# Kernel optimization log

Hardware: AMD Instinct MI355X
Metric: run time of the kernel (lower is better)

The kernel has to match this reference:

```python
import jax, jax.numpy as jnp
import numpy as np
from jax import lax

EPS = 1e-7
MAX_NORM = 1.0 - 1e-5

# ---- Poincare ball (c=1) primitives ----

def _norm(x):
    return jnp.sqrt(jnp.sum(x * x, -1, keepdims=True) + EPS)

def proj(x):
    n = _norm(x)
    return x * jnp.minimum(1.0, MAX_NORM / n)

def expmap0(v):
    n = _norm(v)
    return jnp.tanh(n) * v / n

def logmap0(x):
    n = _norm(x)
    return jnp.arctanh(jnp.clip(n, 0.0, MAX_NORM)) * x / n

def mobius_add(u, v):
    uv = jnp.sum(u * v, -1, keepdims=True)
    uu = jnp.sum(u * u, -1, keepdims=True)
    vv = jnp.sum(v * v, -1, keepdims=True)
    num = (1.0 + 2.0 * uv + vv) * u + (1.0 - uu) * v
    den = 1.0 + 2.0 * uv + uu * vv
    return num / den

# Mobius matvec M (x) x = expmap0(logmap0(x) @ M^T)

def gru_step(h, x, Wr, Wz, Wh, Ur, Uz, Uh, br, bz, bh):
    lh = logmap0(h)
    lx = logmap0(x)
    r = jax.nn.sigmoid(logmap0(mobius_add(mobius_add(expmap0(lh @ Wr.T), expmap0(lx @ Ur.T)), br)))
    z = jax.nn.sigmoid(logmap0(mobius_add(mobius_add(expmap0(lh @ Wz.T), expmap0(lx @ Uz.T)), bz)))
    htil = mobius_add(mobius_add(expmap0((r * lh) @ Wh.T), expmap0(lx @ Uh.T)), bh)
    delta = mobius_add(-h, htil)
    return proj(mobius_add(h, expmap0(z * logmap0(delta))))


def hyperplane_logits(X, P, A):
    # Hyperbolic MLR (Ganea et al.) without materializing [N,V,d]:
    # (-p)(+)x = (-alpha*p + beta*x) / gamma
    xx = jnp.sum(X * X, -1)                  # [N]
    pp = jnp.sum(P * P, -1)                  # [V]
    aa = jnp.sqrt(jnp.sum(A * A, -1) + EPS)  # [V]
    pa = jnp.sum(P * A, -1)                  # [V]
    px = X @ P.T                             # [N,V]
    xa = X @ A.T                             # [N,V]
    alpha = 1.0 - 2.0 * px + xx[:, None]
    beta = (1.0 - pp)[None, :]
    gamma = 1.0 - 2.0 * px + pp[None, :] * xx[:, None]
    da = (-alpha * pa[None, :] + beta * xa) / gamma
    dd = (alpha * alpha * pp[None, :] - 2.0 * alpha * beta * px + beta * beta * xx[:, None]) / (gamma * gamma)
    lam = 2.0 / (1.0 - pp)                   # conformal factor at p_k
    arg = 2.0 * da / ((1.0 - dd) * aa[None, :] + EPS)
    return (lam * aa)[None, :] * jnp.arcsinh(arg)


VOCAB, EMB, HID, LAYERS = 10000, 512, 512, 3
B, S = 16, 128


def setup_inputs() -> dict:
    key = jax.random.key(0)
    ks = jax.random.split(key, 16)
    inp = jax.random.randint(ks[0], (B, S), 0, VOCAB)
    tgt = jax.random.randint(ks[1], (B, S), 0, VOCAB)
    E = proj(0.01 * jax.random.normal(ks[2], (VOCAB, EMB), jnp.float32))
    E = E.at[0].set(0.0)  # padding_idx=0
    mk = lambda k: 0.05 * jax.random.normal(k, (LAYERS, HID, HID), jnp.float32)
    Wr, Wz, Wh = mk(ks[3]), mk(ks[4]), mk(ks[5])
    Ur, Uz, Uh = mk(ks[6]), mk(ks[7]), mk(ks[8])
    mb = lambda k: proj(0.01 * jax.random.normal(k, (LAYERS, HID), jnp.float32))
    br, bz, bh = mb(ks[9]), mb(ks[10]), mb(ks[11])
    P = proj(0.01 * jax.random.normal(ks[12], (VOCAB, HID), jnp.float32))
    A = 0.05 * jax.random.normal(ks[13], (VOCAB, HID), jnp.float32)
    return {"input": inp, "target": tgt, "E": E, "Wr": Wr, "Wz": Wz, "Wh": Wh,
            "Ur": Ur, "Uz": Uz, "Uh": Uh, "br": br, "bz": bz, "bh": bh, "P": P, "A": A}


def reference(input, target, E, Wr, Wz, Wh, Ur, Uz, Uh, br, bz, bh, P, A):
    b, s = input.shape
    x = E[input]                       # [B,S,H] points on the ball
    x = jnp.transpose(x, (1, 0, 2))    # [S,B,H]
    for l in range(LAYERS):
        params = (Wr[l], Wz[l], Wh[l], Ur[l], Uz[l], Uh[l],
                  br[l][None, :], bz[l][None, :], bh[l][None, :])
        def step(h, xt, params=params):
            h = gru_step(h, xt, *params)
            return h, h
        h0 = jnp.zeros((b, HID), x.dtype)
        _, x = lax.scan(step, h0, x)   # [S,B,H]
    X = x.transpose(1, 0, 2).reshape(-1, HID)          # [B*S,H]
    logits = hyperplane_logits(X, P, A)                # [B*S,V]
    logp = jax.nn.log_softmax(logits, axis=-1)
    nll = -jnp.take_along_axis(logp, target.reshape(-1, 1), axis=1)[:, 0]
    return jnp.mean(nll).reshape(1)
```

## Files before the change

kernel.cpp:

```cpp
#include <hip/hip_runtime.h>
#include <hip/hip_bf16.h>
#include <math.h>

#define EPSF 1e-7f
#define MAXNRM 0.99999f

static constexpr int Bb = 16, Ss = 128, Hh = 512, Vv = 10000, Ll = 3;
static constexpr int Nn = Bb * Ss;
static constexpr int VT = 625;

typedef __attribute__((ext_vector_type(4))) float f32x4;
typedef __attribute__((ext_vector_type(8))) short short8v;
typedef _Float16 h2 __attribute__((ext_vector_type(2)));

__device__ inline float4 ld4(const float* p){ return *(const float4*)p; }
__device__ inline void st4(float* p, float4 v){ *(float4*)p = v; }
__device__ inline float dot4(float4 a, float4 b){ return a.x*b.x + a.y*b.y + a.z*b.z + a.w*b.w; }
__device__ inline float sigm(float x){ return 1.f/(1.f + expf(-x)); }
__device__ inline unsigned short f2bf(float f){
  __hip_bfloat16 h = __float2bfloat16(f);
  return __builtin_bit_cast(unsigned short, h);
}
__device__ inline unsigned short f2h(float f){
  _Float16 h = (_Float16)f;
  return __builtin_bit_cast(unsigned short, h);
}
__device__ inline float rsum64f(float v){
  v+=__shfl_xor(v,32); v+=__shfl_xor(v,16); v+=__shfl_xor(v,8);
  v+=__shfl_xor(v,4);  v+=__shfl_xor(v,2);  v+=__shfl_xor(v,1); return v;
}
__device__ inline float dot4_e5m2(uint u, h2 L0, h2 L1, float acc){
  uint p01 = __builtin_amdgcn_perm(u, 0u, 0x05000400u);
  uint p23 = __builtin_amdgcn_perm(u, 0u, 0x07000600u);
  acc = __builtin_amdgcn_fdot2(__builtin_bit_cast(h2,p01), L0, acc, false);
  acc = __builtin_amdgcn_fdot2(__builtin_bit_cast(h2,p23), L1, acc, false);
  return acc;
}
__device__ inline void stg_sc(float* p, float v){
  asm volatile("global_store_dword %0, %1, off sc0 sc1" :: "v"(p), "v"(v) : "memory");
}
__device__ inline float ldg_sc1(const float* p){
  float r;
  asm volatile("global_load_dword %0, %1, off sc0 sc1\n\ts_waitcnt vmcnt(0)"
               : "=v"(r) : "v"(p) : "memory");
  return r;
}

__device__ __forceinline__ void stream_e5m2_pair(const uint* __restrict__ WA,
    const uint* __restrict__ WB, const uint* src2, float (*part)[Hh], int tid, int j8){
  int hf = tid >> 9;
  int kq = (tid >> 6) & 7;
  const uint* W = (hf ? WB : WA) + (size_t)(kq*16)*Hh + j8;
  float acc[8] = {0,0,0,0,0,0,0,0};
  #pragma unroll 4
  for(int i=0;i<16;i++){
    uint4 wa = *(const uint4*)(W + (size_t)i*Hh);
    uint4 wb = *(const uint4*)(W + (size_t)i*Hh + 4);
    uint2 L = *(const uint2*)&src2[(kq*16+i)*2];
    h2 L0=__builtin_bit_cast(h2,L.x), L1=__builtin_bit_cast(h2,L.y);
    acc[0]=dot4_e5m2(wa.x,L0,L1,acc[0]); acc[1]=dot4_e5m2(wa.y,L0,L1,acc[1]);
    acc[2]=dot4_e5m2(wa.z,L0,L1,acc[2]); acc[3]=dot4_e5m2(wa.w,L0,L1,acc[3]);
    acc[4]=dot4_e5m2(wb.x,L0,L1,acc[4]); acc[5]=dot4_e5m2(wb.y,L0,L1,acc[5]);
    acc[6]=dot4_e5m2(wb.z,L0,L1,acc[6]); acc[7]=dot4_e5m2(wb.w,L0,L1,acc[7]);
  }
  float* d = &part[hf*8+kq][j8];
  *(f32x4*)d = (f32x4){acc[0],acc[1],acc[2],acc[3]};
  *(f32x4*)(d+4) = (f32x4){acc[4],acc[5],acc[6],acc[7]};
}
__device__ __forceinline__ void stream_f16_16(const uint* __restrict__ W2, const uint* src2,
    float (*part)[Hh], int tid, int j8){
  int ks = tid >> 6;
  int kp0 = ks*16;
  const uint* W = W2 + (size_t)kp0*Hh + j8;
  f32x4 a0 = {0,0,0,0}, a1 = {0,0,0,0};
  #pragma unroll 4
  for(int kk=0; kk<16; kk++){
    uint4 wa = *(const uint4*)(W + (size_t)kk*Hh);
    uint4 wb = *(const uint4*)(W + (size_t)kk*Hh + 4);
    h2 lv = __builtin_bit_cast(h2, src2[kp0+kk]);
    a0[0]=__builtin_amdgcn_fdot2(__builtin_bit_cast(h2,wa.x), lv, a0[0], false);
    a0[1]=__builtin_amdgcn_fdot2(__builtin_bit_cast(h2,wa.y), lv, a0[1], false);
    a0[2]=__builtin_amdgcn_fdot2(__builtin_bit_cast(h2,wa.z), lv, a0[2], false);
    a0[3]=__builtin_amdgcn_fdot2(__builtin_bit_cast(h2,wa.w), lv, a0[3], false);
    a1[0]=__builtin_amdgcn_fdot2(__builtin_bit_cast(h2,wb.x), lv, a1[0], false);
    a1[1]=__builtin_amdgcn_fdot2(__builtin_bit_cast(h2,wb.y), lv, a1[1], false);
    a1[2]=__builtin_amdgcn_fdot2(__builtin_bit_cast(h2,wb.z), lv, a1[2], false);
    a1[3]=__builtin_amdgcn_fdot2(__builtin_bit_cast(h2,wb.w), lv, a1[3], false);
  }
  float* d = &part[ks][j8];
  *(f32x4*)d = a0; *(f32x4*)(d+4) = a1;
}

__global__ __launch_bounds__(256) void k_packWh(const float* __restrict__ Wh, uint* __restrict__ W2){
  int jt = blockIdx.x, kt2 = blockIdx.y, l = blockIdx.z;
  const float* src = Wh + (size_t)l*Hh*Hh;
  uint* dst = W2 + (size_t)l*(256*Hh);
  __shared__ float t[64][65];
  int tid = threadIdx.x;
  #pragma unroll
  for(int p=0;p<4;p++){
    int row = p*16 + (tid>>4);
    int c4 = (tid&15)*4;
    st4(&t[row][c4], ld4(src + ((size_t)(jt*64+row))*Hh + kt2*64 + c4));
  }
  __syncthreads();
  int kp_l = tid >> 3;
  int j8 = (tid & 7)*8;
  uint u[8];
  #pragma unroll
  for(int i=0;i<8;i++){
    int jl = j8 + i;
    u[i] = (uint)f2h(t[jl][2*kp_l]) | ((uint)f2h(t[jl][2*kp_l+1]) << 16);
  }
  uint* o = dst + (size_t)(kt2*32 + kp_l)*Hh + jt*64 + j8;
  *(uint4*)(o)   = make_uint4(u[0],u[1],u[2],u[3]);
  *(uint4*)(o+4) = make_uint4(u[4],u[5],u[6],u[7]);
}

__global__ __launch_bounds__(256) void k_packW8(const float* __restrict__ Wr,
    const float* __restrict__ Wz, uint* __restrict__ W8){
  int jt = blockIdx.x, kt = blockIdx.y, lm = blockIdx.z;
  int l = lm>>1, m = lm&1;
  const float* src = (m==0?Wr:Wz) + (size_t)l*Hh*Hh;
  uint* dst = W8 + (size_t)lm*(128*Hh);
  __shared__ float t[64][65];
  int tid = threadIdx.x;
  #pragma unroll
  for(int p=0;p<4;p++){
    int row = p*16 + (tid>>4);
    int c4 = (tid&15)*4;
    st4(&t[row][c4], ld4(src + ((size_t)(jt*64+row))*Hh + kt*64 + c4));
  }
  __syncthreads();
  #pragma unroll
  for(int p=0;p<4;p++){
    int k4l = p*4 + (tid>>6);
    int j_l = tid & 63;
    uint u = 0;
    #pragma unroll
    for(int i=0;i<4;i++){
      ushort b16 = __builtin_bit_cast(ushort, (_Float16)t[j_l][k4l*4+i]);
      uint b8 = (uint)((ushort)(b16 + 0x80) >> 8);
      u |= b8 << (8*i);
    }
// ... 69 lines not shown
  float4 v = ld4(Xp + (size_t)n*Hh + t*4);
  float ss = dot4(v,v);
  for(int o=32;o;o>>=1) ss += __shfl_down(ss,o);
  if((t&63)==0) sred[t>>6] = ss;
  __syncthreads();
  ss = sred[0]+sred[1];
  float nn = sqrtf(ss + EPSF);
  float sc = tanhf(nn) / nn;
  v.x*=sc; v.y*=sc; v.z*=sc; v.w*=sc;
  st4(Xp + (size_t)n*Hh + t*4, v);
}

__global__ __launch_bounds__(256) void k_gemm(const float* __restrict__ A4,
    const float* __restrict__ U0, const float* __restrict__ U1, const float* __restrict__ U2,
    float* __restrict__ O0, float* __restrict__ O1, float* __restrict__ O2){
  __shared__ float As[16][65], Bs[16][65];
  int jb = blockIdx.x;
  int nb = blockIdx.y;
  int mat = jb >> 3; int j0 = (jb & 7)*64;
  const float* Bm = mat==0?U0 : (mat==1?U1:U2);
  float* Om       = mat==0?O0 : (mat==1?O1:O2);
  int tid = threadIdx.x;
  int lr = tid >> 2, lq = tid & 3;
  int tx = tid & 15, ty = tid >> 4;
  float acc[4][4] = {};
  for(int kb=0; kb<Hh; kb+=16){
    float4 av = ld4(A4 + (size_t)(nb*64+lr)*Hh + kb + lq*4);
    float4 bv = ld4(Bm + (size_t)(j0+lr)*Hh + kb + lq*4);
    As[lq*4+0][lr]=av.x; As[lq*4+1][lr]=av.y; As[lq*4+2][lr]=av.z; As[lq*4+3][lr]=av.w;
    Bs[lq*4+0][lr]=bv.x; Bs[lq*4+1][lr]=bv.y; Bs[lq*4+2][lr]=bv.z; Bs[lq*4+3][lr]=bv.w;
    __syncthreads();
    #pragma unroll
    for(int kk=0;kk<16;kk++){
      float a0=As[kk][ty*4+0], a1=As[kk][ty*4+1], a2=As[kk][ty*4+2], a3=As[kk][ty*4+3];
      float b0=Bs[kk][tx*4+0], b1=Bs[kk][tx*4+1], b2=Bs[kk][tx*4+2], b3=Bs[kk][tx*4+3];
      acc[0][0]+=a0*b0; acc[0][1]+=a0*b1; acc[0][2]+=a0*b2; acc[0][3]+=a0*b3;
      acc[1][0]+=a1*b0; acc[1][1]+=a1*b1; acc[1][2]+=a1*b2; acc[1][3]+=a1*b3;
      acc[2][0]+=a2*b0; acc[2][1]+=a2*b1; acc[2][2]+=a2*b2; acc[2][3]+=a2*b3;
      acc[3][0]+=a3*b0; acc[3][1]+=a3*b1; acc[3][2]+=a3*b2; acc[3][3]+=a3*b3;
    }
    __syncthreads();
  }
  for(int i=0;i<4;i++)
    for(int j2=0;j2<4;j2++)
      Om[(size_t)(nb*64+ty*4+i)*Hh + j0 + tx*4 + j2] = acc[i][j2];
}

__global__ __launch_bounds__(1024) void k_mega(
    const float* __restrict__ XR, const float* __restrict__ XZ, const float* __restrict__ XH,
    const float* __restrict__ pubX,
    const uint* __restrict__ W8, const uint* __restrict__ W2h,
    const uint* __restrict__ U8, const uint* __restrict__ U2h,
    const float* __restrict__ brA, const float* __restrict__ bzA, const float* __restrict__ bhA,
    float* __restrict__ bnd0, float* __restrict__ bnd1,
    int* __restrict__ flags0, int* __restrict__ flags1,
    float* __restrict__ Xfin){
  const int xcd = blockIdx.x & 7;
  const int layer = xcd >> 1;
  if(layer >= 3) return;
  const int b = (xcd & 1)*8 + (blockIdx.x >> 3);
  const int tid = threadIdx.x;
  const int lane = tid & 63, wv = tid >> 6;
  const int j8 = lane * 8;

  const uint* W8r = W8 + (size_t)(layer*2+0)*128*Hh;
  const uint* W8z = W8 + (size_t)(layer*2+1)*128*Hh;
  const uint* Wh2 = W2h + (size_t)layer*256*Hh;
  const uint* U8r = U8 + (size_t)(layer*2+0)*128*Hh;
  const uint* U8z = U8 + (size_t)(layer*2+1)*128*Hh;
  const uint* Uh2 = U2h + (size_t)layer*256*Hh;
  const float* br = brA + layer*Hh;
  const float* bz = bzA + layer*Hh;
  const float* bh = bhA + layer*Hh;
  float* outX = (layer==0)? bnd0 : (layer==1)? bnd1 : Xfin;
  int* outF = (layer==0)? flags0 : (layer==1)? flags1 : nullptr;
  const float* inX = (layer==1)? bnd0 : bnd1;
  int* inF = (layer==1)? flags0 : flags1;

  __shared__ float part[16][Hh];
  __shared__ float mr_s[Hh], mur_s[Hh];
  __shared__ uint  lh2_s[256], ap2_s[256], lx2_s[256];
  __shared__ float bias0[Hh], bias1[Hh], bias2[Hh];
  __shared__ float partA[8][16];
  __shared__ float partB[8][18];
  __shared__ float coefA_s[12], coefB_s[8], bb_s[4];

  if(tid<256) lh2_s[tid]=0u;
  for(int i=tid;i<Hh;i+=1024){ bias0[i]=br[i]; bias1[i]=bz[i]; bias2[i]=bh[i]; }
  __syncthreads();
  {
    float p0=0,p1=0,p2=0;
    if(tid<Hh){ float a=bias0[tid],b2=bias1[tid],c2=bias2[tid]; p0=a*a; p1=b2*b2; p2=c2*c2; }
    p0=rsum64f(p0); p1=rsum64f(p1); p2=rsum64f(p2);
    if(tid<Hh && lane==0){ partB[wv][0]=p0; partB[wv][1]=p1; partB[wv][2]=p2; }
    __syncthreads();
    if(tid==0){
      float a=0,b2=0,c2=0;
      for(int i=0;i<8;i++){ a+=partB[i][0]; b2+=partB[i][1]; c2+=partB[i][2]; }
      bb_s[0]=a; bb_s[1]=b2; bb_s[2]=c2;
    }
    __syncthreads();
  }

  float h = 0.f;
  float Sh = 0.f, hxh = 0.f, hbh = 0.f;

  for(int ts=0; ts<Ss; ts++){
    const size_t row = (size_t)(ts*Bb + b)*Hh;

    if(layer == 0){
      float xr=0,xz=0,xh=0;
      if(tid<512){ xr=XR[row+tid]; xz=XZ[row+tid]; xh=XH[row+tid]; }
      stream_e5m2_pair(W8r, W8z, lh2_s, part, tid, j8);
      __syncthreads();
      float mr=0.f, mz=0.f;
      if(tid<512){
        float s0=0, s1=0;
        #pragma unroll
        for(int q=0;q<8;q++){ s0+=part[q][tid]; s1+=part[8+q][tid]; }
        mr=s0; mz=s1; mr_s[tid]=s0;
        float brc=bias0[tid], bzc=bias1[tid], bhc=bias2[tid];
        float p0=mr*mr, p1=mr*xr, p2=mr*brc, p3=mz*mz, p4=mz*xz, p5=mz*bzc, p6=h*xh, p7=h*bhc;
        p0=rsum64f(p0); p1=rsum64f(p1); p2=rsum64f(p2); p3=rsum64f(p3);
        p4=rsum64f(p4); p5=rsum64f(p5); p6=rsum64f(p6); p7=rsum64f(p7);
        if(lane==0){
          partA[wv][0]=p0; partA[wv][1]=p1; partA[wv][2]=p2; partA[wv][3]=p3;
          partA[wv][4]=p4; partA[wv][5]=p5; partA[wv][6]=p6; partA[wv][7]=p7;
        }
      }
      __syncthreads();
      if(tid==0){
        float s[8];
        #pragma unroll
        for(int d=0;d<8;d++){
          float x=0;
          for(int i=0;i<8;i++) x+=partA[i][d];
          s[d]=x;
        }
        hxh=s[6]; hbh=s[7];
        const float* px = pubX + (size_t)(ts*Bb+b)*6;
        float xrxr=px[0], xrbr=px[1], xzxz=px[2], xzbz=px[3];
        float bbr=bb_s[0], bbz=bb_s[1];
        float nm=sqrtf(s[0]+EPSF), se=tanhf(nm)/nm;
        float uv=se*s[1], uu=se*se*s[0];
        float den=1.f+2.f*uv+uu*xrxr;
        float a1=(1.f+2.f*uv+xrxr)*se/den, a2=(1.f-uu)/den;
        float uv2=a1*s[2]+a2*xrbr;
        float uu2=a1*a1*s[0]+2.f*a1*a2*s[1]+a2*a2*xrxr;
        float den2=1.f+2.f*uv2+uu2*bbr;
        float b1=(1.f+2.f*uv2+bbr)/den2, b2c=(1.f-uu2)/den2;
        float c1=b1*a1, c2=b1*a2, c3=b2c;
        float n2sq=c1*c1*s[0]+c2*c2*xrxr+c3*c3*bbr+2.f*(c1*c2*s[1]+c1*c3*s[2]+c2*c3*xrbr);
        float nn2=sqrtf(n2sq+EPSF);
        float s_r=atanhf(fminf(nn2,MAXNRM))/nn2;
        coefA_s[0]=s_r*c1; coefA_s[1]=s_r*c2; coefA_s[2]=s_r*c3;
        float nmz=sqrtf(s[3]+EPSF), sez=tanhf(nmz)/nmz;
        float uvz=sez*s[4], uuz=sez*sez*s[3];
        float denz=1.f+2.f*uvz+uuz*xzxz;
        float az1=(1.f+2.f*uvz+xzxz)*sez/denz, az2=(1.f-uuz)/denz;
        float uvz2=az1*s[5]+az2*xzbz;
        float uuz2=az1*az1*s[3]+2.f*az1*az2*s[4]+az2*az2*xzxz;
// ... 51 lines not shown
        float Ghh=dsum[4], Ghm=dsum[5], Ghx=dsum[6], Ghb=dsum[7];
        float Gmm=dsum[8], Gmx=dsum[9], Gmb=dsum[10];
        float Gxx=dsum[11], Gxb=dsum[12], Gbb=dsum[13];
        float Heh=dsum[14], Hem=dsum[15], Hex=dsum[16], Heb=dsum[17];
        float xhxh=coefA_s[7], xhbh=coefA_s[8];
        float bbh=bb_s[2]; float Shb=Sh;
        float nm3=sqrtf(d0+EPSF), se3=tanhf(nm3)/nm3;
        float uvh=se3*d1, uuh=se3*se3*d0;
        float denh=1.f+2.f*uvh+uuh*xhxh;
        float a1p=(1.f+2.f*uvh+xhxh)*se3/denh, a2p=(1.f-uuh)/denh;
        float uv2h=a1p*d2+a2p*xhbh;
        float uu2h=a1p*a1p*d0+2.f*a1p*a2p*d1+a2p*a2p*xhxh;
        float den2h=1.f+2.f*uv2h+uu2h*bbh;
        float b1p=(1.f+2.f*uv2h+bbh)/den2h, b2p=(1.f-uu2h)/den2h;
        float c1p=b1p*a1p, c2p=b1p*a2p, c3p=b2p;
        float h_htil=c1p*d3+c2p*hxh+c3p*hbh;
        float htil2=c1p*c1p*d0+c2p*c2p*xhxh+c3p*c3p*bbh
                  +2.f*(c1p*c2p*d1+c1p*c3p*d2+c2p*c3p*xhbh);
        float denD=1.f-2.f*h_htil+Shb*htil2;
        float dd1=(1.f-2.f*h_htil+htil2)/denD, dd2=(1.f-Shb)/denD;
        float g0=-dd1, g1=dd2*c1p, g2=dd2*c2p, g3=dd2*c3p;
        float del2=g0*g0*Shb+g1*g1*d0+g2*g2*xhxh+g3*g3*bbh
                 +2.f*(g0*g1*d3+g0*g2*hxh+g0*g3*hbh+g1*g2*d1+g1*g3*d2+g2*g3*xhbh);
        float ndl=sqrtf(del2+EPSF);
        float sld=atanhf(fminf(ndl,MAXNRM))/ndl;
        float Qe=g0*g0*Ghh+g1*g1*Gmm+g2*g2*Gxx+g3*g3*Gbb
               +2.f*(g0*g1*Ghm+g0*g2*Ghx+g0*g3*Ghb+g1*g2*Gmx+g1*g3*Gmb+g2*g3*Gxb);
        float Le=g0*Heh+g1*Hem+g2*Hex+g3*Heb;
        float Sww=sld*sld*Qe;
        float Shw=sld*Le;
        float nw=sqrtf(Sww+EPSF), sew=tanhf(nw)/nw;
        float uvw=sew*Shw, vvw=sew*sew*Sww;
        float denw=1.f+2.f*uvw+Shb*vvw;
        float q1=(1.f+2.f*uvw+vvw)/denw, q2=((1.f-Shb)/denw)*sew;
        float n2h=q1*q1*Shb+2.f*q1*q2*Shw+q2*q2*Sww;
        float nrm=sqrtf(n2h+EPSF);
        float scl=fminf(1.f, MAXNRM/nrm);
        float Shn=scl*scl*n2h;
        float nh2=sqrtf(Shn+EPSF);
        float slh=atanhf(fminf(nh2,MAXNRM))/nh2;
        coefB_s[0]=scl*q1; coefB_s[1]=scl*q2*sld;
        coefB_s[2]=g0; coefB_s[3]=g1; coefB_s[4]=g2; coefB_s[5]=g3;
        coefB_s[6]=slh;
        Sh=Shn;
      }
      __syncthreads();
      if(tid<512){
        float qc1=coefB_s[0], qc2=coefB_s[1];
        float g0=coefB_s[2], g1=coefB_s[3], g2=coefB_s[4], g3=coefB_s[5];
        float slh=coefB_s[6];
        float dl = g0*h + g1*mh + g2*xh + g3*bias2[tid];
        float hn = qc1*h + qc2*z*dl;
        h = hn;
        stg_sc(outX + row + tid, hn);
        float lh = slh*hn;
        float lhp = __shfl_xor(lh, 1);
        if(!(tid&1)) lh2_s[tid>>1] = (uint)f2h(lh) | ((uint)f2h(lhp)<<16);
      }
      __syncthreads();
      if(tid==0) __hip_atomic_store(outF + b*Ss + ts, 1, __ATOMIC_RELAXED, __HIP_MEMORY_SCOPE_AGENT);
    } else {
      stream_e5m2_pair(W8r, W8z, lh2_s, part, tid, j8);
      __syncthreads();
      float mr=0.f, mz=0.f;
      if(tid<512){
        float s0=0, s1=0;
        #pragma unroll
        for(int q=0;q<8;q++){ s0+=part[q][tid]; s1+=part[8+q][tid]; }
        mr=s0; mz=s1; mr_s[tid]=s0;
        float brc=bias0[tid], bzc=bias1[tid];
        float p0=mr*mr, p1=mr*brc, p2=mz*mz, p3=mz*bzc;
        p0=rsum64f(p0); p1=rsum64f(p1); p2=rsum64f(p2); p3=rsum64f(p3);
        if(lane==0){ partA[wv][0]=p0; partA[wv][1]=p1; partA[wv][2]=p2; partA[wv][3]=p3; }
      }
      if(tid==0){
        while(__hip_atomic_load(inF + b*Ss + ts, __ATOMIC_RELAXED, __HIP_MEMORY_SCOPE_AGENT) == 0)
          __builtin_amdgcn_s_sleep(1);
      }
      __syncthreads();
      float x = 0.f;
      if(tid<512){
        x = ldg_sc1(inX + row + tid);
        float p4 = rsum64f(x*x);
        if(lane==0) partA[wv][4]=p4;
      }
      __syncthreads();
      if(tid<512){
        float xx=0;
        #pragma unroll
        for(int i=0;i<8;i++) xx+=partA[i][4];
        float n=sqrtf(xx+EPSF);
        float slx=atanhf(fminf(n,MAXNRM))/n;
        float lx = slx*x;
        float lxp = __shfl_xor(lx, 1);
        if(!(tid&1)) lx2_s[tid>>1] = (uint)f2h(lx) | ((uint)f2h(lxp)<<16);
      }
      __syncthreads();
      stream_e5m2_pair(U8r, U8z, lx2_s, part, tid, j8);
      __syncthreads();
      float mur=0.f, muz=0.f;
      if(tid<512){
        float s0=0, s1=0;
        #pragma unroll
        for(int q=0;q<8;q++){ s0+=part[q][tid]; s1+=part[8+q][tid]; }
        mur=s0; muz=s1; mur_s[tid]=s0;
        float brc=bias0[tid], bzc=bias1[tid];
        float p5=mur*mur, p6=mur*brc, p7=muz*muz, p8=muz*bzc, p9=mr*mur, p10=mz*muz;
        p5=rsum64f(p5); p6=rsum64f(p6); p7=rsum64f(p7);
        p8=rsum64f(p8); p9=rsum64f(p9); p10=rsum64f(p10);
        if(lane==0){
          partA[wv][5]=p5; partA[wv][6]=p6; partA[wv][7]=p7;
          partA[wv][8]=p8; partA[wv][9]=p9; partA[wv][10]=p10;
        }
      }
      __syncthreads();
      stream_f16_16(Uh2, lx2_s, part, tid, j8);
      __syncthreads();
      float muh=0.f;
      if(tid<512){
        float s=0;
        #pragma unroll
        for(int q=0;q<16;q++) s+=part[q][tid];
        muh=s;
        float bhc=bias2[tid];
        float p11=muh*muh, p12=h*muh, p13=muh*bhc, p14=h*bhc;
        p11=rsum64f(p11); p12=rsum64f(p12); p13=rsum64f(p13); p14=rsum64f(p14);
        if(lane==0){ partA[wv][11]=p11; partA[wv][12]=p12; partA[wv][13]=p13; partA[wv][14]=p14; }
      }
      __syncthreads();
      if(tid==0){
        float S[15];
        #pragma unroll
        for(int d=0;d<15;d++){
          float xS=0;
          for(int i=0;i<8;i++) xS+=partA[i][d];
          S[d]=xS;
        }
        float bbr=bb_s[0], bbz=bb_s[1];
        float nur=sqrtf(S[5]+EPSF), se_r=tanhf(nur)/nur;
        float nuz=sqrtf(S[7]+EPSF), se_z=tanhf(nuz)/nuz;
        float nuh=sqrtf(S[11]+EPSF), se_h=tanhf(nuh)/nuh;
        float s0=S[0], s1=se_r*S[9], s2=S[1];
        float xrxr=se_r*se_r*S[5], xrbr=se_r*S[6];
        float s3=S[2], s4=se_z*S[10], s5=S[3];
        float xzxz=se_z*se_z*S[7], xzbz=se_z*S[8];
        hxh = se_h*S[12]; hbh = S[14];
        float xhxh=se_h*se_h*S[11], xhbh=se_h*S[13];
        float nm=sqrtf(s0+EPSF), se=tanhf(nm)/nm;
        float uv=se*s1, uu=se*se*s0;
        float den=1.f+2.f*uv+uu*xrxr;
        float a1=(1.f+2.f*uv+xrxr)*se/den, a2=(1.f-uu)/den;
        float uv2=a1*s2+a2*xrbr;
        float uu2=a1*a1*s0+2.f*a1*a2*s1+a2*a2*xrxr;
        float den2=1.f+2.f*uv2+uu2*bbr;
        float b1=(1.f+2.f*uv2+bbr)/den2, b2c=(1.f-uu2)/den2;
        float c1=b1*a1, c2=b1*a2, c3=b2c;
        float n2sq=c1*c1*s0+c2*c2*xrxr+c3*c3*bbr+2.f*(c1*c2*s1+c1*c3*s2+c2*c3*xrbr);
        float nn2=sqrtf(n2sq+EPSF);
        float s_r=atanhf(fminf(nn2,MAXNRM))/nn2;
        coefA_s[0]=s_r*c1; coefA_s[1]=s_r*c2*se_r; coefA_s[2]=s_r*c3;
        float nmz=sqrtf(s3+EPSF), sez=tanhf(nmz)/nmz;
        float uvz=sez*s4, uuz=sez*sez*s3;
        float denz=1.f+2.f*uvz+uuz*xzxz;
        float az1=(1.f+2.f*uvz+xzxz)*sez/denz, az2=(1.f-uuz)/denz;
        float uvz2=az1*s5+az2*xzbz;
        float uuz2=az1*az1*s3+2.f*az1*az2*s4+az2*az2*xzxz;
        float denz2=1.f+2.f*uvz2+uuz2*bbz;
        float bz1=(1.f+2.f*uvz2+bbz)/denz2, bz2=(1.f-uuz2)/denz2;
        float cz1=bz1*az1, cz2=bz1*az2, cz3=bz2;
        float nz2sq=cz1*cz1*s3+cz2*cz2*xzxz+cz3*cz3*bbz+2.f*(cz1*cz2*s4+cz1*cz3*s5+cz2*cz3*xzbz);
        float nnz2=sqrtf(nz2sq+EPSF);
        float s_z=atanhf(fminf(nnz2,MAXNRM))/nnz2;
        coefA_s[3]=s_z*cz1; coefA_s[4]=s_z*cz2*se_z; coefA_s[5]=s_z*cz3;
        coefA_s[6]=se_h; coefA_s[7]=xhxh; coefA_s[8]=xhbh;
      }
      __syncthreads();
      if(tid<256){
        int e0 = tid*2;
        float ca=coefA_s[0], cbp=coefA_s[1], cc2=coefA_s[2];
        h2 lp = __builtin_bit_cast(h2, lh2_s[tid]);
        float r0 = sigm(ca*mr_s[e0]   + cbp*mur_s[e0]   + cc2*bias0[e0]);
        float r1 = sigm(ca*mr_s[e0+1] + cbp*mur_s[e0+1] + cc2*bias0[e0+1]);
        ap2_s[tid] = (uint)f2h(r0*(float)lp[0]) | ((uint)f2h(r1*(float)lp[1])<<16);
      }
      __syncthreads();
      stream_f16_16(Wh2, ap2_s, part, tid, j8);
      __syncthreads();
      float mh=0.f, z=0.f;
      if(tid<512){
        float s=0;
        #pragma unroll
        for(int q=0;q<16;q++) s+=part[q][tid];
        mh=s;
        float se_h = coefA_s[6];
        float xh = se_h*muh;
        float bhc=bias2[tid], bzc=bias1[tid];
        z = sigm(coefA_s[3]*mz + coefA_s[4]*muz + coefA_s[5]*bzc);
        float eh=z*h, em=z*mh, ex=z*xh, eb=z*bhc;
        float p[18] = {mh*mh, mh*xh, mh*bhc, h*mh,
                       eh*eh, eh*em, eh*ex, eh*eb,
                       em*em, em*ex, em*eb, ex*ex, ex*eb, eb*eb,
                       h*eh, h*em, h*ex, h*eb};
        #pragma unroll
        for(int d=0;d<18;d++) p[d]=rsum64f(p[d]);
        if(lane==0){
          #pragma unroll
          for(int d=0;d<18;d++) partB[wv][d]=p[d];
        }
      }
      __syncthreads();
      if(tid==0){
        float dsum[18];
        #pragma unroll
        for(int d=0;d<18;d++){
          float xS=0;
          for(int i=0;i<8;i++) xS+=partB[i][d];
          dsum[d]=xS;
        }
        float d0=dsum[0], d1=dsum[1], d2=dsum[2], d3=dsum[3];
        float Ghh=dsum[4], Ghm=dsum[5], Ghx=dsum[6], Ghb=dsum[7];
        float Gmm=dsum[8], Gmx=dsum[9], Gmb=dsum[10];
        float Gxx=dsum[11], Gxb=dsum[12], Gbb=dsum[13];
        float Heh=dsum[14], Hem=dsum[15], Hex=dsum[16], Heb=dsum[17];
        float xhxh=coefA_s[7], xhbh=coefA_s[8];
        float bbh=bb_s[2]; float Shb=Sh;
        float nm3=sqrtf(d0+EPSF), se3=tanhf(nm3)/nm3;
        float uvh=se3*d1, uuh=se3*se3*d0;
        float denh=1.f+2.f*uvh+uuh*xhxh;
        float a1p=(1.f+2.f*uvh+xhxh)*se3/denh, a2p=(1.f-uuh)/denh;
        float uv2h=a1p*d2+a2p*xhbh;
        float uu2h=a1p*a1p*d0+2.f*a1p*a2p*d1+a2p*a2p*xhxh;
        float den2h=1.f+2.f*uv2h+uu2h*bbh;
        float b1p=(1.f+2.f*uv2h+bbh)/den2h, b2p=(1.f-uu2h)/den2h;
        float c1p=b1p*a1p, c2p=b1p*a2p, c3p=b2p;
        float h_htil=c1p*d3+c2p*hxh+c3p*hbh;
        float htil2=c1p*c1p*d0+c2p*c2p*xhxh+c3p*c3p*bbh
                  +2.f*(c1p*c2p*d1+c1p*c3p*d2+c2p*c3p*xhbh);
        float denD=1.f-2.f*h_htil+Shb*htil2;
        float dd1=(1.f-2.f*h_htil+htil2)/denD, dd2=(1.f-Shb)/denD;
        float g0=-dd1, g1=dd2*c1p, g2=dd2*c2p, g3=dd2*c3p;
        float del2=g0*g0*Shb+g1*g1*d0+g2*g2*xhxh+g3*g3*bbh
                 +2.f*(g0*g1*d3+g0*g2*hxh+g0*g3*hbh+g1*g2*d1+g1*g3*d2+g2*g3*xhbh);
        float ndl=sqrtf(del2+EPSF);
        float sld=atanhf(fminf(ndl,MAXNRM))/ndl;
        float Qe=g0*g0*Ghh+g1*g1*Gmm+g2*g2*Gxx+g3*g3*Gbb
               +2.f*(g0*g1*Ghm+g0*g2*Ghx+g0*g3*Ghb+g1*g2*Gmx+g1*g3*Gmb+g2*g3*Gxb);
        float Le=g0*Heh+g1*Hem+g2*Hex+g3*Heb;
        float Sww=sld*sld*Qe;
        float Shw=sld*Le;
        float nw=sqrtf(Sww+EPSF), sew=tanhf(nw)/nw;
        float uvw=sew*Shw, vvw=sew*sew*Sww;
        float denw=1.f+2.f*uvw+Shb*vvw;
        float q1=(1.f+2.f*uvw+vvw)/denw, q2=((1.f-Shb)/denw)*sew;
        float n2h=q1*q1*Shb+2.f*q1*q2*Shw+q2*q2*Sww;
        float nrm=sqrtf(n2h+EPSF);
        float scl=fminf(1.f, MAXNRM/nrm);
        float Shn=scl*scl*n2h;
        float nh2=sqrtf(Shn+EPSF);
        float slh=atanhf(fminf(nh2,MAXNRM))/nh2;
        coefB_s[0]=scl*q1; coefB_s[1]=scl*q2*sld;
        coefB_s[2]=g0; coefB_s[3]=g1; coefB_s[4]=g2; coefB_s[5]=g3;
        coefB_s[6]=slh;
        Sh=Shn;
      }
      __syncthreads();
      if(tid<512){
        float qc1=coefB_s[0], qc2=coefB_s[1];
        float g0=coefB_s[2], g1=coefB_s[3], g2=coefB_s[4], g3=coefB_s[5];
        float slh=coefB_s[6];
        float xh = coefA_s[6]*muh;
        float dl = g0*h + g1*mh + g2*xh + g3*bias2[tid];
        float hn = qc1*h + qc2*z*dl;
        h = hn;
        if(layer==1) stg_sc(outX + row + tid, hn);
        else Xfin[row + tid] = hn;
        float lh = slh*hn;
        float lhp = __shfl_xor(lh, 1);
        if(!(tid&1)) lh2_s[tid>>1] = (uint)f2h(lh) | ((uint)f2h(lhp)<<16);
      }
      __syncthreads();
      if(layer==1 && tid==0)
        __hip_atomic_store(outF + b*Ss + ts, 1, __ATOMIC_RELAXED, __HIP_MEMORY_SCOPE_AGENT);
    }
  }
}

__global__ __launch_bounds__(256) void k_packF(const float* __restrict__ src, ushort* __restrict__ dst){
  int vt = blockIdx.x;
  __shared__ float rows[16][516];
  int tid = threadIdx.x;
  #pragma unroll
  for(int p=0;p<8;p++){
    int idx = p*256 + tid;
    int row = idx >> 7, c4 = idx & 127;
    st4(&rows[row][c4*4], ld4(src + ((size_t)vt*16+row)*Hh + c4*4));
  }
  __syncthreads();
  #pragma unroll
  for(int p=0;p<4;p++){
    int idx = p*256 + tid;
    int kt = idx >> 6, lane = idx & 63;
    int vloc = lane & 15, k0 = kt*32 + ((lane>>4)&3)*8;
    union { ushort u[8]; uint4 v; } tt;
    #pragma unroll
    for(int i=0;i<8;i++) tt.u[i] = f2bf(rows[vloc][k0+i]);
    *(uint4*)(dst + (((size_t)vt*16 + kt)*64 + lane)*8) = tt.v;
  }
}

__global__ __launch_bounds__(256) void k_mlr2(
    const ushort* __restrict__ Xf, const ushort* __restrict__ Pf, const ushort* __restrict__ Af,
    const float* __restrict__ X, const float* __restrict__ pp, const float* __restrict__ aa,
    const float* __restrict__ pa, const int* __restrict__ tgt,
    float* __restrict__ pm, float* __restrict__ tl){
  int rb = blockIdx.x;
  int sp = blockIdx.y;
  int tid = threadIdx.x, lane = tid&63, w = tid>>6;
  __shared__ ushort Axf[4*16*64*8];
  __shared__ float xxp[64][4];
  __shared__ float xxs[64];
  #pragma unroll
  for(int p=0;p<16;p++){
    int idx = p*256 + tid;
    ((uint4*)Axf)[idx] = ((const uint4*)Xf)[(size_t)rb*4096 + idx];
  }
  {
    int row = tid>>2, seg = tid&3;
    const float* xr = X + ((size_t)rb*64 + row)*Hh + seg*128;
    float s=0;
    #pragma unroll
    for(int i=0;i<32;i++){ float4 v4 = ld4(xr+i*4); s += dot4(v4,v4); }
// ... 73 lines not shown
        int idx=rt*4+i;
        int rr = rb*64 + rt*16 + (lane>>4)*4 + i;
        pm[((size_t)rr*32 + sp*4 + w)*2+0] = mM[idx];
        pm[((size_t)rr*32 + sp*4 + w)*2+1] = sS[idx];
      }
  }
}

__global__ void k_final(const float* __restrict__ pm, const float* __restrict__ tl, float* __restrict__ out){
  int tid = threadIdx.x;
  __shared__ float sred[4];
  float acc = 0.f;
  for(int q=0;q<8;q++){
    int rr = q*256 + tid;
    float M = -3.0e38f;
    for(int s=0;s<32;s++) M = fmaxf(M, pm[((size_t)rr*32+s)*2]);
    float Ssum = 0.f;
    for(int s=0;s<32;s++) Ssum += pm[((size_t)rr*32+s)*2+1]*expf(pm[((size_t)rr*32+s)*2]-M);
    acc += (M + logf(Ssum)) - tl[rr];
  }
  for(int o=32;o;o>>=1) acc += __shfl_down(acc,o);
  if((tid&63)==0) sred[tid>>6] = acc;
  __syncthreads();
  if(tid==0) out[0] = (sred[0]+sred[1]+sred[2]+sred[3]) / 2048.f;
}

extern "C" void kernel_launch(void* const* d_in, const int* in_sizes, int n_in,
                              void* d_out, int out_size, void* d_ws, size_t ws_size,
                              hipStream_t stream){
  const int* inp = (const int*)d_in[0];
  const int* tgt = (const int*)d_in[1];
  const float* E  = (const float*)d_in[2];
  const float* Wr = (const float*)d_in[3];
  const float* Wz = (const float*)d_in[4];
  const float* Wh = (const float*)d_in[5];
  const float* Ur = (const float*)d_in[6];
  const float* Uz = (const float*)d_in[7];
  const float* Uh = (const float*)d_in[8];
  const float* br = (const float*)d_in[9];
  const float* bz = (const float*)d_in[10];
  const float* bh = (const float*)d_in[11];
  const float* P  = (const float*)d_in[12];
  const float* A  = (const float*)d_in[13];
  float* out = (float*)d_out;
  float* w = (float*)d_ws;
  size_t o = 0;
  auto take = [&](size_t n){ float* p = w + o; o += n; return p; };
  float* Xa  = take((size_t)Nn*Hh);
  float* Xb  = take((size_t)Nn*Hh);
  float* LX  = take((size_t)Nn*Hh);
  float* XR  = take((size_t)Nn*Hh);
  float* XZ  = take((size_t)Nn*Hh);
  float* XH  = take((size_t)Nn*Hh);
  float* BD1 = take((size_t)Nn*Hh);
  uint*  W2h = (uint*)take((size_t)3*256*Hh);
  uint*  W8  = (uint*)take((size_t)6*128*Hh);
  uint*  U2h = (uint*)take((size_t)3*256*Hh);
  uint*  U8  = (uint*)take((size_t)6*128*Hh);
  float* pubX = take((size_t)Nn*6);
  float* pp  = take(10240);
  float* aa  = take(10240);
  float* pa  = take(10240);
  float* pm  = take((size_t)Nn*32*2);
  float* tl  = take((size_t)Nn);
  int* flags = (int*)take(2*(size_t)Bb*Ss);
  if(ws_size < o*sizeof(float)) return;
  int* flags0 = flags;
  int* flags1 = flags + Bb*Ss;

  hipLaunchKernelGGL(k_packWh, dim3(8,8,3), dim3(256), 0, stream, Wh, W2h);
  hipLaunchKernelGGL(k_packWh, dim3(8,8,3), dim3(256), 0, stream, Uh, U2h);
  hipLaunchKernelGGL(k_packW8, dim3(8,8,6), dim3(256), 0, stream, Wr, Wz, W8);
  hipLaunchKernelGGL(k_packW8, dim3(8,8,6), dim3(256), 0, stream, Ur, Uz, U8);
  hipLaunchKernelGGL(k_pav, dim3(2500), dim3(256), 0, stream, P,A, pp,aa,pa);
  hipLaunchKernelGGL(k_embed, dim3(Nn), dim3(128), 0, stream, inp, E, Xa);
  hipLaunchKernelGGL(k_logmap, dim3(Nn), dim3(128), 0, stream, Xa, LX);
  hipLaunchKernelGGL(k_gemm, dim3(24,32), dim3(256), 0, stream, LX,
                     Ur, Uz, Uh, XR, XZ, XH);
  hipLaunchKernelGGL(k_expmap, dim3(Nn,3), dim3(128), 0, stream, XR,XZ,XH);
  hipLaunchKernelGGL(k_predots, dim3(Nn), dim3(128), 0, stream, XR,XZ,XH, br, bz, bh, pubX);
  hipMemsetAsync(flags, 0, 2*(size_t)Bb*Ss*sizeof(int), stream);
  hipLaunchKernelGGL(k_mega, dim3(64), dim3(1024), 0, stream,
                     XR,XZ,XH, pubX, W8,W2h,U8,U2h, br,bz,bh,
                     LX , BD1, flags0, flags1, Xb);
  ushort* Pf = (ushort*)LX;
  ushort* Af = Pf + (size_t)VT*16*64*8;
  ushort* Xf = (ushort*)Xa;
  hipLaunchKernelGGL(k_packF, dim3(VT), dim3(256), 0, stream, P, Pf);
  hipLaunchKernelGGL(k_packF, dim3(VT), dim3(256), 0, stream, A, Af);
  hipLaunchKernelGGL(k_packF, dim3(128), dim3(256), 0, stream, Xb, Xf);
  hipLaunchKernelGGL(k_mlr2, dim3(32,8), dim3(256), 0, stream, Xf, Pf, Af, Xb,
                     pp, aa, pa, tgt, pm, tl);
  hipLaunchKernelGGL(k_final, dim3(1), dim3(256), 0, stream, pm, tl, out);
}
```

Measured before the change: 4.516 ms.

## Pass packed fp16 logmap across layers and overlap W/U streams in GRU megakernel

The producing layer now writes its logmapped hidden state as packed fp16 pairs, which the consumer loads straight into lx2_s. This drops the consumer's reload of fp32 h, its norm reduction, the atanh and the extra barriers. Wave groups are specialized so the W-recurrent matvec runs on half the block while the other half waits on the flag and loads the boundary, and later U matvecs overlap with reductions. This shortens the per-timestep critical path and halves the boundary traffic, at the cost of relying on the fp16 logmap from the previous layer and an uneven work split.

```diff
diff --git a/kernel.cpp b/kernel.cpp
--- a/kernel.cpp
+++ b/kernel.cpp
@@ -36,11 +36,11 @@
   acc = __builtin_amdgcn_fdot2(__builtin_bit_cast(h2,p23), L1, acc, false);
   return acc;
 }
-__device__ inline void stg_sc(float* p, float v){
+__device__ inline void stg_scu(uint* p, uint v){
   asm volatile("global_store_dword %0, %1, off sc0 sc1" :: "v"(p), "v"(v) : "memory");
 }
-__device__ inline float ldg_sc1(const float* p){
-  float r;
+__device__ inline uint ldg_scu(const uint* p){
+  uint r;
   asm volatile("global_load_dword %0, %1, off sc0 sc1\n\ts_waitcnt vmcnt(0)"
                : "=v"(r) : "v"(p) : "memory");
   return r;
@@ -64,6 +64,26 @@
     acc[6]=dot4_e5m2(wb.z,L0,L1,acc[6]); acc[7]=dot4_e5m2(wb.w,L0,L1,acc[7]);
   }
   float* d = &part[hf*8+kq][j8];
+  *(f32x4*)d = (f32x4){acc[0],acc[1],acc[2],acc[3]};
+  *(f32x4*)(d+4) = (f32x4){acc[4],acc[5],acc[6],acc[7]};
+}
+__device__ __forceinline__ void stream_e5m2_q(const uint* __restrict__ W8m,
+    const uint* src2, float (*part)[Hh], int unit, int lane, int prow){
+  const int j8 = lane*8;
+  const uint* W = W8m + (size_t)(unit*32)*Hh + j8;
+  float acc[8] = {0,0,0,0,0,0,0,0};
+  #pragma unroll 4
+  for(int i=0;i<32;i++){
+    uint4 wa = *(const uint4*)(W + (size_t)i*Hh);
+    uint4 wb = *(const uint4*)(W + (size_t)i*Hh + 4);
+    uint2 L = *(const uint2*)&src2[(unit*32+i)*2];
+    h2 L0=__builtin_bit_cast(h2,L.x), L1=__builtin_bit_cast(h2,L.y);
+    acc[0]=dot4_e5m2(wa.x,L0,L1,acc[0]); acc[1]=dot4_e5m2(wa.y,L0,L1,acc[1]);
+    acc[2]=dot4_e5m2(wa.z,L0,L1,acc[2]); acc[3]=dot4_e5m2(wa.w,L0,L1,acc[3]);
+    acc[4]=dot4_e5m2(wb.x,L0,L1,acc[4]); acc[5]=dot4_e5m2(wb.y,L0,L1,acc[5]);
+    acc[6]=dot4_e5m2(wb.z,L0,L1,acc[6]); acc[7]=dot4_e5m2(wb.w,L0,L1,acc[7]);
+  }
+  float* d = &part[prow][j8];
   *(f32x4*)d = (f32x4){acc[0],acc[1],acc[2],acc[3]};
   *(f32x4*)(d+4) = (f32x4){acc[4],acc[5],acc[6],acc[7]};
 }
@@ -90,6 +110,28 @@
   float* d = &part[ks][j8];
   *(f32x4*)d = a0; *(f32x4*)(d+4) = a1;
 }
+__device__ __forceinline__ void stream_f16_e(const uint* __restrict__ W2m, const uint* src2,
+    float (*part)[Hh], int unit, int lane, int prow){
+  const int j8 = lane*8;
+  const uint* W = W2m + (size_t)(unit*32)*Hh + j8;
+  f32x4 a0 = {0,0,0,0}, a1 = {0,0,0,0};
+  #pragma unroll 4
+  for(int kk=0; kk<32; kk++){
+    uint4 wa = *(const uint4*)(W + (size_t)kk*Hh);
+    uint4 wb = *(const uint4*)(W + (size_t)kk*Hh + 4);
+    h2 lv = __builtin_bit_cast(h2, src2[unit*32+kk]);
+    a0[0]=__builtin_amdgcn_fdot2(__builtin_bit_cast(h2,wa.x), lv, a0[0], false);
+    a0[1]=__builtin_amdgcn_fdot2(__builtin_bit_cast(h2,wa.y), lv, a0[1], false);
+    a0[2]=__builtin_amdgcn_fdot2(__builtin_bit_cast(h2,wa.z), lv, a0[2], false);
+    a0[3]=__builtin_amdgcn_fdot2(__builtin_bit_cast(h2,wa.w), lv, a0[3], false);
+    a1[0]=__builtin_amdgcn_fdot2(__builtin_bit_cast(h2,wb.x), lv, a1[0], false);
+    a1[1]=__builtin_amdgcn_fdot2(__builtin_bit_cast(h2,wb.y), lv, a1[1], false);
+    a1[2]=__builtin_amdgcn_fdot2(__builtin_bit_cast(h2,wb.z), lv, a1[2], false);
+    a1[3]=__builtin_amdgcn_fdot2(__builtin_bit_cast(h2,wb.w), lv, a1[3], false);
+  }
+  float* d = &part[prow][j8];
+  *(f32x4*)d = a0; *(f32x4*)(d+4) = a1;
+}
 
 __global__ __launch_bounds__(256) void k_packWh(const float* __restrict__ Wh, uint* __restrict__ W2){
   int jt = blockIdx.x, kt2 = blockIdx.y, l = blockIdx.z;
@@ -265,7 +307,7 @@
     const uint* __restrict__ W8, const uint* __restrict__ W2h,
     const uint* __restrict__ U8, const uint* __restrict__ U2h,
     const float* __restrict__ brA, const float* __restrict__ bzA, const float* __restrict__ bhA,
-    float* __restrict__ bnd0, float* __restrict__ bnd1,
+    uint* __restrict__ LH0, uint* __restrict__ LH1,
     int* __restrict__ flags0, int* __restrict__ flags1,
     float* __restrict__ Xfin){
   const int xcd = blockIdx.x & 7;
@@ -285,13 +327,13 @@
   const float* br = brA + layer*Hh;
   const float* bz = bzA + layer*Hh;
   const float* bh = bhA + layer*Hh;
-  float* outX = (layer==0)? bnd0 : (layer==1)? bnd1 : Xfin;
+  uint* outLH = (layer==0)? LH0 : (layer==1)? LH1 : nullptr;
   int* outF = (layer==0)? flags0 : (layer==1)? flags1 : nullptr;
-  const float* inX = (layer==1)? bnd0 : bnd1;
+  const uint* inLH = (layer==1)? LH0 : LH1;
   int* inF = (layer==1)? flags0 : flags1;
 
   __shared__ float part[16][Hh];
-  __shared__ float mr_s[Hh], mur_s[Hh];
+  __shared__ float mr_s[Hh], mz_s[Hh], mur_s[Hh], muz_s[Hh];
   __shared__ uint  lh2_s[256], ap2_s[256], lx2_s[256];
   __shared__ float bias0[Hh], bias1[Hh], bias2[Hh];
   __shared__ float partA[8][16];
@@ -320,6 +362,7 @@
 
   for(int ts=0; ts<Ss; ts++){
     const size_t row = (size_t)(ts*Bb + b)*Hh;
+    const size_t lrow = (size_t)(ts*Bb + b)*256;
 
     if(layer == 0){
       float xr=0,xz=0,xh=0;
@@ -477,75 +520,65 @@
         float dl = g0*h + g1*mh + g2*xh + g3*bias2[tid];
         float hn = qc1*h + qc2*z*dl;
         h = hn;
-        stg_sc(outX + row + tid, hn);
         float lh = slh*hn;
         float lhp = __shfl_xor(lh, 1);
-        if(!(tid&1)) lh2_s[tid>>1] = (uint)f2h(lh) | ((uint)f2h(lhp)<<16);
+        if(!(tid&1)){
+          uint pk = (uint)f2h(lh) | ((uint)f2h(lhp)<<16);
+          lh2_s[tid>>1] = pk;
+          stg_scu(outLH + lrow + (tid>>1), pk);
+        }
       }
       __syncthreads();
       if(tid==0) __hip_atomic_store(outF + b*Ss + ts, 1, __ATOMIC_RELAXED, __HIP_MEMORY_SCOPE_AGENT);
     } else {
-      stream_e5m2_pair(W8r, W8z, lh2_s, part, tid, j8);
-      __syncthreads();
+      if(tid < 512){
+        if(wv < 4) stream_e5m2_q(W8r, lh2_s, part, wv, lane, wv);
+        else       stream_e5m2_q(W8z, lh2_s, part, wv-4, lane, wv);
+      } else if(tid < 768){
+        int idx = tid - 512;
+        while(__hip_atomic_load(inF + b*Ss + ts, __ATOMIC_RELAXED, __HIP_MEMORY_SCOPE_AGENT) == 0)
+          __builtin_amdgcn_s_sleep(1);
+        lx2_s[idx] = ldg_scu(inLH + lrow + idx);
+      }
+      __syncthreads();
+
       float mr=0.f, mz=0.f;
-      if(tid<512){
-        float s0=0, s1=0;
-        #pragma unroll
-        for(int q=0;q<8;q++){ s0+=part[q][tid]; s1+=part[8+q][tid]; }
-        mr=s0; mz=s1; mr_s[tid]=s0;
-        float brc=bias0[tid], bzc=bias1[tid];
-        float p0=mr*mr, p1=mr*brc, p2=mz*mz, p3=mz*bzc;
+      if(tid < 512){
+        mr = part[0][tid]+part[1][tid]+part[2][tid]+part[3][tid];
+        mz = part[4][tid]+part[5][tid]+part[6][tid]+part[7][tid];
+        mr_s[tid]=mr; mz_s[tid]=mz;
+        float p0=mr*mr, p1=mr*bias0[tid], p2=mz*mz, p3=mz*bias1[tid];
         p0=rsum64f(p0); p1=rsum64f(p1); p2=rsum64f(p2); p3=rsum64f(p3);
         if(lane==0){ partA[wv][0]=p0; partA[wv][1]=p1; partA[wv][2]=p2; partA[wv][3]=p3; }
-      }
-      if(tid==0){
-        while(__hip_atomic_load(inF + b*Ss + ts, __ATOMIC_RELAXED, __HIP_MEMORY_SCOPE_AGENT) == 0)
-          __builtin_amdgcn_s_sleep(1);
-      }
-      __syncthreads();
-      float x = 0.f;
-      if(tid<512){
-        x = ldg_sc1(inX + row + tid);
-        float p4 = rsum64f(x*x);
-        if(lane==0) partA[wv][4]=p4;
-      }
-      __syncthreads();
-      if(tid<512){
-        float xx=0;
-        #pragma unroll
-        for(int i=0;i<8;i++) xx+=partA[i][4];
-        float n=sqrtf(xx+EPSF);
-        float slx=atanhf(fminf(n,MAXNRM))/n;
-        float lx = slx*x;
-        float lxp = __shfl_xor(lx, 1);
-        if(!(tid&1)) lx2_s[tid>>1] = (uint)f2h(lx) | ((uint)f2h(lxp)<<16);
-      }
-      __syncthreads();
-      stream_e5m2_pair(U8r, U8z, lx2_s, part, tid, j8);
-      __syncthreads();
-      float mur=0.f, muz=0.f;
-      if(tid<512){
-        float s0=0, s1=0;
-        #pragma unroll
-        for(int q=0;q<8;q++){ s0+=part[q][tid]; s1+=part[8+q][tid]; }
-        mur=s0; muz=s1; mur_s[tid]=s0;
-        float brc=bias0[tid], bzc=bias1[tid];
-        float p5=mur*mur, p6=mur*brc, p7=muz*muz, p8=muz*bzc, p9=mr*mur, p10=mz*muz;
+      } else {
+        if(wv < 12) stream_e5m2_q(U8r, lx2_s, part, wv-8, lane, wv);
+        else        stream_e5m2_q(U8z, lx2_s, part, wv-12, lane, wv);
+      }
+      __syncthreads();
+
+      if(tid < 512){
+        stream_f16_e(Uh2, lx2_s, part, wv, lane, wv);
+      } else {
+        int j = tid - 512;
+        float mur = part[8][j]+part[9][j]+part[10][j]+part[11][j];
+        float muz = part[12][j]+part[13][j]+part[14][j]+part[15][j];
+        mur_s[j]=mur; muz_s[j]=muz;
+        float p5=mur*mur, p6=mur*bias0[j], p7=muz*muz, p8=muz*bias1[j];
+        float p9=mr_s[j]*mur, p10=mz_s[j]*muz;
         p5=rsum64f(p5); p6=rsum64f(p6); p7=rsum64f(p7);
         p8=rsum64f(p8); p9=rsum64f(p9); p10=rsum64f(p10);
         if(lane==0){
-          partA[wv][5]=p5; partA[wv][6]=p6; partA[wv][7]=p7;
-          partA[wv][8]=p8; partA[wv][9]=p9; partA[wv][10]=p10;
+          partA[wv-8][5]=p5; partA[wv-8][6]=p6; partA[wv-8][7]=p7;
+          partA[wv-8][8]=p8; partA[wv-8][9]=p9; partA[wv-8][10]=p10;
         }
       }
       __syncthreads();
-      stream_f16_16(Uh2, lx2_s, part, tid, j8);
-      __syncthreads();
+
       float muh=0.f;
       if(tid<512){
         float s=0;
         #pragma unroll
-        for(int q=0;q<16;q++) s+=part[q][tid];
+        for(int q=0;q<8;q++) s+=part[q][tid];
         muh=s;
         float bhc=bias2[tid];
         float p11=muh*muh, p12=h*muh, p13=muh*bhc, p14=h*bhc;
@@ -553,6 +586,7 @@
         if(lane==0){ partA[wv][11]=p11; partA[wv][12]=p12; partA[wv][13]=p13; partA[wv][14]=p14; }
       }
       __syncthreads();
+
       if(tid==0){
         float S[15];
         #pragma unroll
@@ -600,6 +634,7 @@
         coefA_s[6]=se_h; coefA_s[7]=xhxh; coefA_s[8]=xhbh;
       }
       __syncthreads();
+
       if(tid<256){
         int e0 = tid*2;
         float ca=coefA_s[0], cbp=coefA_s[1], cc2=coefA_s[2];
@@ -609,8 +644,10 @@
         ap2_s[tid] = (uint)f2h(r0*(float)lp[0]) | ((uint)f2h(r1*(float)lp[1])<<16);
       }
       __syncthreads();
+
       stream_f16_16(Wh2, ap2_s, part, tid, j8);
       __syncthreads();
+
       float mh=0.f, z=0.f;
       if(tid<512){
         float s=0;
@@ -620,7 +657,7 @@
         float se_h = coefA_s[6];
         float xh = se_h*muh;
         float bhc=bias2[tid], bzc=bias1[tid];
-        z = sigm(coefA_s[3]*mz + coefA_s[4]*muz + coefA_s[5]*bzc);
+        z = sigm(coefA_s[3]*mz + coefA_s[4]*muz_s[tid] + coefA_s[5]*bzc);
         float eh=z*h, em=z*mh, ex=z*xh, eb=z*bhc;
         float p[18] = {mh*mh, mh*xh, mh*bhc, h*mh,
                        eh*eh, eh*em, eh*ex, eh*eb,
@@ -634,6 +671,7 @@
         }
       }
       __syncthreads();
+
       if(tid==0){
         float dsum[18];
         #pragma unroll
@@ -689,6 +727,7 @@
         Sh=Shn;
       }
       __syncthreads();
+
       if(tid<512){
         float qc1=coefB_s[0], qc2=coefB_s[1];
         float g0=coefB_s[2], g1=coefB_s[3], g2=coefB_s[4], g3=coefB_s[5];
@@ -697,11 +736,14 @@
         float dl = g0*h + g1*mh + g2*xh + g3*bias2[tid];
         float hn = qc1*h + qc2*z*dl;
         h = hn;
-        if(layer==1) stg_sc(outX + row + tid, hn);
-        else Xfin[row + tid] = hn;
+        if(layer==2) Xfin[row + tid] = hn;
         float lh = slh*hn;
         float lhp = __shfl_xor(lh, 1);
-        if(!(tid&1)) lh2_s[tid>>1] = (uint)f2h(lh) | ((uint)f2h(lhp)<<16);
+        if(!(tid&1)){
+          uint pk = (uint)f2h(lh) | ((uint)f2h(lhp)<<16);
+          lh2_s[tid>>1] = pk;
+          if(layer==1) stg_scu(outLH + lrow + (tid>>1), pk);
+        }
       }
       __syncthreads();
       if(layer==1 && tid==0)
@@ -881,7 +923,8 @@
   float* XR  = take((size_t)Nn*Hh);
   float* XZ  = take((size_t)Nn*Hh);
   float* XH  = take((size_t)Nn*Hh);
-  float* BD1 = take((size_t)Nn*Hh);
+  uint*  LH0 = (uint*)take((size_t)Nn*256);
+  uint*  LH1 = (uint*)take((size_t)Nn*256);
   uint*  W2h = (uint*)take((size_t)3*256*Hh);
   uint*  W8  = (uint*)take((size_t)6*128*Hh);
   uint*  U2h = (uint*)take((size_t)3*256*Hh);
@@ -911,7 +954,7 @@
   hipMemsetAsync(flags, 0, 2*(size_t)Bb*Ss*sizeof(int), stream);
   hipLaunchKernelGGL(k_mega, dim3(64), dim3(1024), 0, stream,
                      XR,XZ,XH, pubX, W8,W2h,U8,U2h, br,bz,bh,
-                     LX , BD1, flags0, flags1, Xb);
+                     LH0, LH1, flags0, flags1, Xb);
   ushort* Pf = (ushort*)LX;
   ushort* Af = Pf + (size_t)VT*16*64*8;
   ushort* Xf = (ushort*)Xa;
```

Result: faster. 4.354 ms (-3.6%).
